# Optimization experiments

Measured on AMD Instinct MI355X. Metric: run time of the kernel, lower is better.

Reference implementation:

```python
import jax, jax.numpy as jnp
import numpy as np


def setup_inputs() -> dict:
    key = jax.random.key(0)
    k1, k2, k3, k4 = jax.random.split(key, 4)
    S, B, I, H = 2048, 64, 512, 512
    stdv = 1.0 / np.sqrt(H)
    x = jax.random.normal(k1, (S, B, I), dtype=jnp.float32)
    W = jax.random.uniform(k2, (I, 4 * H), dtype=jnp.float32, minval=-stdv, maxval=stdv)
    U = jax.random.uniform(k3, (H, 4 * H), dtype=jnp.float32, minval=-stdv, maxval=stdv)
    bias = jax.random.uniform(k4, (4 * H,), dtype=jnp.float32, minval=-stdv, maxval=stdv)
    return {"x": x, "W": W, "U": U, "bias": bias}


def reference(x, W, U, bias):
    # x: [S, B, I] (batch_first=False). Gates order: i, f, g, o.
    S, B, I = x.shape
    H = U.shape[0]
    # Precompute input projection for all timesteps (batched GEMM).
    xW = jnp.einsum('sbi,ig->sbg', x, W) + bias  # [S, B, 4H]

    def step(carry, xw_t):
        h, c = carry
        gates = xw_t + h @ U  # [B, 4H]
        i_t = jax.nn.sigmoid(gates[:, :H])
        f_t = jax.nn.sigmoid(gates[:, H:2 * H])
        g_t = jnp.tanh(gates[:, 2 * H:3 * H])
        o_t = jax.nn.sigmoid(gates[:, 3 * H:])
        c_new = f_t * c + i_t * g_t
        h_new = o_t * jnp.tanh(c_new)
        return (h_new, c_new), h_new

    h0 = jnp.zeros((B, H), dtype=x.dtype)
    c0 = jnp.zeros((B, H), dtype=x.dtype)
    (h_t, c_t), hidden_seq = jax.lax.scan(step, (h0, c0), xW)
    return hidden_seq, (h_t, c_t)
```

## Files before the change

kernel.cpp:

```cpp
#include <hip/hip_runtime.h>
#include <hip/hip_bf16.h>

#define SLEN 2048
#define BROWS 64
#define IDIM 512
#define HDIM 512
#define BH (BROWS * HDIM)
#define RING 32
#define HRING 8
#define NREC 64
#define NTOT 256
#define NTHREADS 512

typedef __bf16 bf16x8 __attribute__((ext_vector_type(8)));
typedef float  f32x4  __attribute__((ext_vector_type(4)));
typedef int    i32x4  __attribute__((ext_vector_type(4)));
typedef int    i32x2  __attribute__((ext_vector_type(2)));

__device__ inline unsigned short f2bf(float f) {
  union { float f; unsigned u; } v; v.f = f;
  unsigned r = v.u + 0x7FFFu + ((v.u >> 16) & 1u);
  return (unsigned short)(r >> 16);
}
__device__ inline float bf2f(unsigned short s) {
  union { unsigned u; float f; } v; v.u = ((unsigned)s) << 16;
  return v.f;
}
__device__ inline float sigm(float x) {
  return __builtin_amdgcn_rcpf(1.f + __expf(-x));
}
__device__ inline float tanh_f(float x) {
  float e = __expf(2.f * x);
  return 1.f - 2.f * __builtin_amdgcn_rcpf(e + 1.f);
}

__global__ __launch_bounds__(256) void prep_ct(const float* __restrict__ W,
                                               const float* __restrict__ U,
                                               unsigned short* __restrict__ CT) {
  int k = blockIdx.x;
  const float* src = (k < IDIM) ? (W + (size_t)k * 2048) : (U + (size_t)(k - IDIM) * 2048);
  for (int j = threadIdx.x; j < 2048; j += 256) {
    int gate = j >> 9, hcol = j & 511;
    int w = hcol >> 5, n = (hcol >> 2) & 7, hsub = hcol & 3;
    int row = w * 128 + n * 16 + gate * 4 + hsub;
    CT[(size_t)row * 1024 + k] = f2bf(src[j]);
  }
}

__global__ __launch_bounds__(NTHREADS)
void lstm_fused(const float* __restrict__ x, const float* __restrict__ bias,
                const unsigned short* __restrict__ CT,
                unsigned short* __restrict__ gring,
                unsigned short* __restrict__ hG,
                unsigned* __restrict__ flags,
                unsigned* __restrict__ flags2,
                float* __restrict__ out) {
  const int bid  = blockIdx.x;
  const int tid  = threadIdx.x;
  const int lane = tid & 63;
  const int wid  = tid >> 6;
  const int lg   = lane >> 4;
  const int lc   = lane & 15;

  extern __shared__ char Udyn[];
  __shared__ union {
    struct {
      unsigned short Ast[16 * 512];
      unsigned short Gst[16 * 128];
      unsigned short stag[16][32];
    } r;
    unsigned short Gout[64 * 128];
  } sm;

  if (bid >= NREC) {
    const int wid2 = bid - NREC;
    const int w2 = wid2 & 15;
    const int s  = wid2 >> 4;
    const int rt = wid & 3;
    const int ch = wid >> 2;

    float bias_v[4];
    #pragma unroll
    for (int c4 = 0; c4 < 4; ++c4) {
      int n2 = 4 * ch + c4;
      bias_v[c4] = bias[(lc >> 2) * 512 + w2 * 32 + n2 * 4 + (lc & 3)];
    }

    for (int t = s; t < SLEN; t += 12) {
      if (wid == 0 && t >= RING) {
        unsigned need = (unsigned)(t - RING + 2);
        const unsigned* bp = flags + (size_t)((lane & 3) * 16 + w2) * 16;
        while (__ballot((lane < 4) &&
                        (__hip_atomic_load(bp, __ATOMIC_RELAXED,
                                           __HIP_MEMORY_SCOPE_AGENT) < need)) != 0ull)
          __builtin_amdgcn_s_sleep(16);
      }

      f32x4 acc[4];
      #pragma unroll
      for (int c4 = 0; c4 < 4; ++c4)
        acc[c4] = (f32x4){bias_v[c4], bias_v[c4], bias_v[c4], bias_v[c4]};

      const float* xp = x + ((size_t)t * BROWS + 16 * rt + lc) * IDIM + lg * 8;
      #pragma unroll
      for (int kk = 0; kk < 16; ++kk) {
        f32x4 v0 = *(const f32x4*)(xp + kk * 32);
        f32x4 v1 = *(const f32x4*)(xp + kk * 32 + 4);
        bf16x8 a;
        #pragma unroll
        for (int j = 0; j < 4; ++j) { a[j] = (__bf16)v0[j]; a[4 + j] = (__bf16)v1[j]; }
        #pragma unroll
        for (int c4 = 0; c4 < 4; ++c4) {
          const bf16x8 b = *(const bf16x8*)(CT + (size_t)(w2 * 128 + (4 * ch + c4) * 16 + lc) * 1024
                                            + kk * 32 + lg * 8);
          acc[c4] = __builtin_amdgcn_mfma_f32_16x16x32_bf16(a, b, acc[c4], 0, 0, 0);
        }
      }

      #pragma unroll
      for (int c4 = 0; c4 < 4; ++c4)
        #pragma unroll
        for (int reg = 0; reg < 4; ++reg)
          sm.Gout[(size_t)(16 * rt + 4 * lg + reg) * 128 + (4 * ch + c4) * 16 + lc]
            = f2bf(acc[c4][reg]);
      __syncthreads();

      {
        int row = tid >> 3, cs = (tid & 7) * 16;
        const unsigned short* srcp = sm.Gout + (size_t)row * 128 + cs;
        i32x4 v0 = *(const i32x4*)srcp;
        i32x4 v1 = *(const i32x4*)(srcp + 8);
        unsigned short* d = gring + (size_t)(t & (RING - 1)) * (BROWS * 2048)
                          + (size_t)row * 2048 + w2 * 128 + cs;
        asm volatile("global_store_dwordx4 %0, %1, off sc1" :: "v"(d), "v"(v0) : "memory");
        asm volatile("global_store_dwordx4 %0, %1, off offset:16 sc1" :: "v"(d), "v"(v1) : "memory");
        asm volatile("s_waitcnt vmcnt(0)" ::: "memory");
      }
      __syncthreads();
      if (tid == 0)
        __hip_atomic_store(flags2 + (size_t)((t & (RING - 1)) * 16 + w2) * 16,
                           (unsigned)(t + 1), __ATOMIC_RELAXED, __HIP_MEMORY_SCOPE_AGENT);
    }
    return;
  }

  const int g = bid & 3;
  const int w = bid >> 2;
  const int n = wid;

  #pragma unroll
  for (int i = 0; i < 16; ++i) {
    int idx16 = tid + NTHREADS * i;
    int r = idx16 >> 6, c16 = idx16 & 63;
    i32x4 v = *(const i32x4*)(CT + (size_t)(w * 128 + r) * 1024 + 512 + c16 * 8);
    *(i32x4*)(Udyn + (size_t)r * 1024 + ((c16 * 16) ^ ((r & 7) << 4))) = v;
  }
  __syncthreads();

  float cst[4] = {0.f, 0.f, 0.f, 0.f};
  const bool act = (lc < 4);
  const int hcol = w * 32 + n * 4 + (lc & 3);
  const size_t HS = (size_t)SLEN * BH;

  const int prow = tid >> 5;
  const int pc16 = (tid * 2) & 63;

  for (int t = 0; t < SLEN; ++t) {
    {
      const unsigned* fpG = flags2 + (size_t)((t & (RING - 1)) * 16 + w) * 16;
      while (__ballot(__hip_atomic_load(fpG, __ATOMIC_RELAXED,
                                        __HIP_MEMORY_SCOPE_AGENT)
                      <= (unsigned)t) != 0ull) {}
    }

    i32x2 gv;
    {
      const unsigned short* gpG = gring + (size_t)(t & (RING - 1)) * (BROWS * 2048)
                                + ((size_t)16 * g + prow) * 2048 + w * 128 + (tid & 31) * 4;
      asm volatile("global_load_dwordx2 %0, %1, off sc1" : "=&v"(gv) : "v"(gpG) : "memory");
    }
    if (t > 0) {
      const unsigned short* hp = hG + (size_t)((t - 1) & (HRING - 1)) * BH
                               + ((size_t)16 * g + prow) * HDIM + pc16 * 8;
      i32x4 v0, v1;
      int bad;
      do {
        asm volatile("global_load_dwordx4 %0, %2, off sc1\n\t"
                     "global_load_dwordx4 %1, %2, off offset:16 sc1\n\t"
                     "s_waitcnt vmcnt(0)"
                     : "=&v"(v0), "=&v"(v1) : "v"(hp) : "memory");
        bad = 0;
        #pragma unroll
        for (int j = 0; j < 4; ++j) {
          unsigned a = (unsigned)v0[j], b = (unsigned)v1[j];
          bad |= (int)(((a & 0xFFFFu) == 0xFFFFu) | ((a >> 16) == 0xFFFFu)
                     | ((b & 0xFFFFu) == 0xFFFFu) | ((b >> 16) == 0xFFFFu));
        }
      } while (bad);
      int rs = (prow & 7) << 4;
      char* rowb = (char*)sm.r.Ast + prow * 1024;
      *(i32x4*)(rowb + ((pc16 * 16) ^ rs)) = v0;
      *(i32x4*)(rowb + (((pc16 + 1) * 16) ^ rs)) = v1;
    } else {
      asm volatile("s_waitcnt vmcnt(0)" ::: "memory");
    }
    *(i32x2*)(sm.r.Gst + (size_t)prow * 128 + (tid & 31) * 4) = gv;

    if (wid == 0 && lane == 0)
      __hip_atomic_store(flags + (size_t)(g * 16 + w) * 16, (unsigned)(t + 1),
                         __ATOMIC_RELAXED, __HIP_MEMORY_SCOPE_AGENT);

    if (wid == 0 && t >= 2) {
      int row = lane >> 2, ch4 = lane & 3;
      unsigned short* dr = hG + (size_t)((t - 2) & (HRING - 1)) * BH
                         + ((size_t)16 * g + row) * HDIM + w * 32 + ch4 * 8;
      i32x4 ff = {-1, -1, -1, -1};
      asm volatile("global_store_dwordx4 %0, %1, off sc1" :: "v"(dr), "v"(ff) : "memory");
    }
    __syncthreads();

    f32x4 acc;
    #pragma unroll
    for (int reg = 0; reg < 4; ++reg)
      acc[reg] = bf2f(sm.r.Gst[(size_t)(4 * lg + reg) * 128 + n * 16 + lc]);

    if (t > 0) {
      const int sw = (lc & 7) << 4;
      const char* Ab = (const char*)sm.r.Ast + (size_t)lc * 1024;
      const char* Bb = Udyn + (size_t)(n * 16 + lc) * 1024;
      #pragma unroll
      for (int kk = 0; kk < 16; ++kk) {
        int koff = kk * 64 + lg * 16;
        bf16x8 a = *(const bf16x8*)(Ab + (koff ^ sw));
        bf16x8 b = *(const bf16x8*)(Bb + (koff ^ sw));
        acc = __builtin_amdgcn_mfma_f32_16x16x32_bf16(a, b, acc, 0, 0, 0);
      }
    }

    float hnv[4], cnv[4];
    #pragma unroll
    for (int reg = 0; reg < 4; ++reg) {
      float own = acc[reg];
      float g4  = __shfl_xor(own, 4, 64);
      float g8  = __shfl_xor(own, 8, 64);
      float g12 = __shfl_xor(own, 12, 64);
      float it = sigm(own), ft = sigm(g4), gt = tanh_f(g8), ot = sigm(g12);
      float cn = ft * cst[reg] + it * gt;
      cst[reg] = cn;
      float hn = ot * tanh_f(cn);
      hnv[reg] = hn; cnv[reg] = cn;
      if (act) sm.r.stag[4 * lg + reg][n * 4 + (lc & 3)] = f2bf(hn);
    }
    __syncthreads();

    if (t + 1 < SLEN && wid == 0) {
      int row = lane >> 2, ch4 = lane & 3;
      i32x4 hv = *(const i32x4*)((const char*)sm.r.stag + row * 64 + ch4 * 16);
      const unsigned short* d0 = hG + (size_t)(t & (HRING - 1)) * BH
                               + ((size_t)16 * g + row) * HDIM + w * 32 + ch4 * 8;
      asm volatile("global_store_dwordx4 %0, %1, off sc1"
                   :: "v"(d0), "v"(hv) : "memory");
    }

    if (act) {
      #pragma unroll
      for (int reg = 0; reg < 4; ++reg) {
        size_t bglob = (size_t)16 * g + 4 * lg + reg;
        out[(size_t)t * BH + bglob * HDIM + hcol] = hnv[reg];
        if (t == SLEN - 1) {
          out[HS + bglob * HDIM + hcol] = hnv[reg];
          out[HS + BH + bglob * HDIM + hcol] = cnv[reg];
        }
      }
    }
  }
}

extern "C" void kernel_launch(void* const* d_in, const int* in_sizes, int n_in,
                              void* d_out, int out_size, void* d_ws, size_t ws_size,
                              hipStream_t stream) {
  const float* x    = (const float*)d_in[0];
  const float* W    = (const float*)d_in[1];
  const float* U    = (const float*)d_in[2];
  const float* bias = (const float*)d_in[3];
  float* out = (float*)d_out;

  char* p = (char*)d_ws;
  unsigned short* CT    = (unsigned short*)p;  p += (size_t)2048 * 1024 * 2;
  unsigned short* gring = (unsigned short*)p;  p += (size_t)RING * BROWS * 2048 * 2;
  unsigned short* hG    = (unsigned short*)p;  p += (size_t)HRING * BH * 2;
  unsigned* flags  = (unsigned*)p;             p += 4 * 16 * 16 * 4;
  unsigned* flags2 = (unsigned*)p;

  hipMemsetAsync(hG, 0xFF, (size_t)HRING * BH * 2, stream);
  hipMemsetAsync(flags, 0, (4 * 16 + RING * 16) * 16 * sizeof(unsigned), stream);
  prep_ct<<<1024, 256, 0, stream>>>(W, U, CT);
  lstm_fused<<<NTOT, NTHREADS, 128 * 1024, stream>>>(x, bias, CT, gring, hG, flags, flags2, out);
}
```

Measured before the change: 6.026 ms.

## Prefetch next step's input-projection gates alongside h load in recurrent loop

Double-buffers the staged input-projection gate tile in LDS and fetches step t+1's gate slice and its ready flag in the same polling loop that waits for h(t-1). This takes the separate flag-spin and gate load off the critical path of each recurrent step. The flag published to the producer blocks is advanced by one to match the shifted consumption, which changes the ring back-pressure protocol. A step-0 prologue loads the first tile before the loop.

Result: no change. 5.953 ms (-1.2%).

```diff
diff --git a/kernel.cpp b/kernel.cpp
--- a/kernel.cpp
+++ b/kernel.cpp
@@ -66,7 +66,7 @@
   __shared__ union {
     struct {
       unsigned short Ast[16 * 512];
-      unsigned short Gst[16 * 128];
+      unsigned short Gst[2][16 * 128];
       unsigned short stag[16][32];
     } r;
     unsigned short Gout[64 * 128];
@@ -155,6 +155,23 @@
     i32x4 v = *(const i32x4*)(CT + (size_t)(w * 128 + r) * 1024 + 512 + c16 * 8);
     *(i32x4*)(Udyn + (size_t)r * 1024 + ((c16 * 16) ^ ((r & 7) << 4))) = v;
   }
+
+  const int prow = tid >> 5;
+  const int pcol = (tid & 31) * 4;
+  const int pc16 = (tid * 2) & 63;
+
+  {
+    const unsigned* fpG = flags2 + (size_t)(0 * 16 + w) * 16;
+    const unsigned short* gpG = gring + ((size_t)16 * g + prow) * 2048 + w * 128 + pcol;
+    unsigned f2v; i32x2 gv;
+    do {
+      asm volatile("global_load_dword %0, %2, off sc1\n\t"
+                   "global_load_dwordx2 %1, %3, off sc1\n\t"
+                   "s_waitcnt vmcnt(0)"
+                   : "=&v"(f2v), "=&v"(gv) : "v"(fpG), "v"(gpG) : "memory");
+    } while (f2v == 0u);
+    *(i32x2*)(&sm.r.Gst[0][(size_t)prow * 128 + pcol]) = gv;
+  }
   __syncthreads();
 
   float cst[4] = {0.f, 0.f, 0.f, 0.f};
@@ -162,52 +179,52 @@
   const int hcol = w * 32 + n * 4 + (lc & 3);
   const size_t HS = (size_t)SLEN * BH;
 
-  const int prow = tid >> 5;
-  const int pc16 = (tid * 2) & 63;
-
   for (int t = 0; t < SLEN; ++t) {
     {
-      const unsigned* fpG = flags2 + (size_t)((t & (RING - 1)) * 16 + w) * 16;
-      while (__ballot(__hip_atomic_load(fpG, __ATOMIC_RELAXED,
-                                        __HIP_MEMORY_SCOPE_AGENT)
-                      <= (unsigned)t) != 0ull) {}
-    }
-
-    i32x2 gv;
-    {
-      const unsigned short* gpG = gring + (size_t)(t & (RING - 1)) * (BROWS * 2048)
-                                + ((size_t)16 * g + prow) * 2048 + w * 128 + (tid & 31) * 4;
-      asm volatile("global_load_dwordx2 %0, %1, off sc1" : "=&v"(gv) : "v"(gpG) : "memory");
-    }
-    if (t > 0) {
+      const int s = t + 1;
+      const bool ng = (s < SLEN);
+      const unsigned* fpG = flags2 + (size_t)((s & (RING - 1)) * 16 + w) * 16;
+      const unsigned short* gpG = gring + (size_t)(s & (RING - 1)) * (BROWS * 2048)
+                                + ((size_t)16 * g + prow) * 2048 + w * 128 + pcol;
       const unsigned short* hp = hG + (size_t)((t - 1) & (HRING - 1)) * BH
                                + ((size_t)16 * g + prow) * HDIM + pc16 * 8;
-      i32x4 v0, v1;
+      unsigned f2v = 0u; i32x2 gv; i32x4 v0, v1;
       int bad;
       do {
-        asm volatile("global_load_dwordx4 %0, %2, off sc1\n\t"
-                     "global_load_dwordx4 %1, %2, off offset:16 sc1\n\t"
-                     "s_waitcnt vmcnt(0)"
-                     : "=&v"(v0), "=&v"(v1) : "v"(hp) : "memory");
+        if (ng)
+          asm volatile("global_load_dword %0, %2, off sc1\n\t"
+                       "global_load_dwordx2 %1, %3, off sc1"
+                       : "=&v"(f2v), "=&v"(gv) : "v"(fpG), "v"(gpG) : "memory");
+        if (t > 0)
+          asm volatile("global_load_dwordx4 %0, %2, off sc1\n\t"
+                       "global_load_dwordx4 %1, %2, off offset:16 sc1\n\t"
+                       "s_waitcnt vmcnt(0)"
+                       : "=&v"(v0), "=&v"(v1) : "v"(hp) : "memory");
+        else
+          asm volatile("s_waitcnt vmcnt(0)" ::: "memory");
         bad = 0;
-        #pragma unroll
-        for (int j = 0; j < 4; ++j) {
-          unsigned a = (unsigned)v0[j], b = (unsigned)v1[j];
-          bad |= (int)(((a & 0xFFFFu) == 0xFFFFu) | ((a >> 16) == 0xFFFFu)
-                     | ((b & 0xFFFFu) == 0xFFFFu) | ((b >> 16) == 0xFFFFu));
+        if (t > 0) {
+          #pragma unroll
+          for (int j = 0; j < 4; ++j) {
+            unsigned a = (unsigned)v0[j], b = (unsigned)v1[j];
+            bad |= (int)(((a & 0xFFFFu) == 0xFFFFu) | ((a >> 16) == 0xFFFFu)
+                       | ((b & 0xFFFFu) == 0xFFFFu) | ((b >> 16) == 0xFFFFu));
+          }
         }
+        if (ng) bad |= (int)(f2v <= (unsigned)s);
       } while (bad);
-      int rs = (prow & 7) << 4;
-      char* rowb = (char*)sm.r.Ast + prow * 1024;
-      *(i32x4*)(rowb + ((pc16 * 16) ^ rs)) = v0;
-      *(i32x4*)(rowb + (((pc16 + 1) * 16) ^ rs)) = v1;
-    } else {
-      asm volatile("s_waitcnt vmcnt(0)" ::: "memory");
-    }
-    *(i32x2*)(sm.r.Gst + (size_t)prow * 128 + (tid & 31) * 4) = gv;
+
+      if (t > 0) {
+        int rs = (prow & 7) << 4;
+        char* rowb = (char*)sm.r.Ast + prow * 1024;
+        *(i32x4*)(rowb + ((pc16 * 16) ^ rs)) = v0;
+        *(i32x4*)(rowb + (((pc16 + 1) * 16) ^ rs)) = v1;
+      }
+      if (ng) *(i32x2*)(&sm.r.Gst[s & 1][(size_t)prow * 128 + pcol]) = gv;
+    }
 
     if (wid == 0 && lane == 0)
-      __hip_atomic_store(flags + (size_t)(g * 16 + w) * 16, (unsigned)(t + 1),
+      __hip_atomic_store(flags + (size_t)(g * 16 + w) * 16, (unsigned)(t + 2),
                          __ATOMIC_RELAXED, __HIP_MEMORY_SCOPE_AGENT);
 
     if (wid == 0 && t >= 2) {
@@ -222,7 +239,7 @@
     f32x4 acc;
     #pragma unroll
     for (int reg = 0; reg < 4; ++reg)
-      acc[reg] = bf2f(sm.r.Gst[(size_t)(4 * lg + reg) * 128 + n * 16 + lc]);
+      acc[reg] = bf2f(sm.r.Gst[t & 1][(size_t)(4 * lg + reg) * 128 + n * 16 + lc]);
 
     if (t > 0) {
       const int sw = (lc & 7) << 4;
```
